# Performance work log

Measured on AMD Instinct MI355X. Metric: run time of the kernel, lower is better.

Reference implementation:

```python
import jax, jax.numpy as jnp
import numpy as np

C = 768      # n_embd
H = 12       # n_head
L = 6        # n_layer (per stack: base and head)
BS = 256     # block_size (per-stream length t)
B = 2        # batch
VU = 512     # vocab_size_up
VD = 512     # vocab_size_down
NM = 438     # n_music


def _ln(x, g, b, eps=1e-5):
    m = jnp.mean(x, -1, keepdims=True)
    v = jnp.mean((x - m) ** 2, -1, keepdims=True)
    return (x - m) * jax.lax.rsqrt(v + eps) * g + b


def _blocks(x, p, mask):
    # p: tuple of 16 stacked [L, ...] param arrays; scan over layers
    def body(x, lp):
        g1, b1, Wq, Bq, Wk, Bk, Wv, Bv, Wo, Bo, g2, b2, Wf, Bf, Wp, Bp = lp
        Bb, T, Cc = x.shape
        D = Cc // H
        h = _ln(x, g1, b1)
        q = (h @ Wq + Bq).reshape(Bb, T, H, D).transpose(0, 2, 1, 3)
        k = (h @ Wk + Bk).reshape(Bb, T, H, D).transpose(0, 2, 1, 3)
        v = (h @ Wv + Bv).reshape(Bb, T, H, D).transpose(0, 2, 1, 3)
        att = jnp.einsum('bhid,bhjd->bhij', q, k) * (1.0 / np.sqrt(D).astype(np.float32))
        att = jnp.where(mask, att, jnp.float32(-1e9))
        att = jax.nn.softmax(att, axis=-1)
        y = jnp.einsum('bhij,bhjd->bhid', att, v).transpose(0, 2, 1, 3).reshape(Bb, T, Cc)
        x = x + y @ Wo + Bo
        h2 = _ln(x, g2, b2)
        x = x + jax.nn.gelu(h2 @ Wf + Bf, approximate=False) @ Wp + Bp
        return x, None
    x, _ = jax.lax.scan(body, x, p)
    return x


def _forward(idx_up, idx_down, cond, tok_emb_up, tok_emb_down, pos_emb, cond_w, cond_b,
             base_p, head_p, ln_f_g, ln_f_b, head_up_w, head_down_w):
    t = idx_up.shape[1]
    te = jnp.concatenate([cond @ cond_w + cond_b, tok_emb_up[idx_up], tok_emb_down[idx_down]], axis=1)
    pe = jnp.concatenate([pos_emb[:, :t], pos_emb[:, BS:BS + t], pos_emb[:, 2 * BS:2 * BS + t]], axis=1)
    x = te + pe  # [B, 3t, C]
    tril = jnp.tril(jnp.ones((t, t), bool))
    mask = jnp.tile(tril, (3, 3))[None, None]  # 3x3 tiled block-causal mask [1,1,3t,3t]
    x = _blocks(x, base_p, mask)
    x = _blocks(x, head_p, mask)
    x = _ln(x, ln_f_g, ln_f_b)
    logits_up = x[:, t:2 * t] @ head_up_w
    logits_down = x[:, 2 * t:3 * t] @ head_down_w
    return logits_up, logits_down


def setup_inputs() -> dict:
    key = jax.random.key(0)
    ks = iter(jax.random.split(key, 100))
    def nrm(shape):
        return 0.02 * jax.random.normal(next(ks), shape, jnp.float32)
    inp = {
        'idx_up': jax.random.randint(next(ks), (B, BS), 0, VU),
        'idx_down': jax.random.randint(next(ks), (B, BS), 0, VD),
        'cond': jax.random.normal(next(ks), (B, BS, NM), jnp.float32),
        'tok_emb_up': nrm((VU, C)),
        'tok_emb_down': nrm((VD, C)),
        'pos_emb': nrm((1, 3 * BS, C)),
        'cond_w': nrm((NM, C)),
        'cond_b': jnp.zeros((C,), jnp.float32),
    }
    for pre in ('base_', 'head_'):
        inp[pre + 'ln1_g'] = jnp.ones((L, C), jnp.float32)
        inp[pre + 'ln1_b'] = jnp.zeros((L, C), jnp.float32)
        inp[pre + 'wq'] = nrm((L, C, C)); inp[pre + 'bq'] = jnp.zeros((L, C), jnp.float32)
        inp[pre + 'wk'] = nrm((L, C, C)); inp[pre + 'bk'] = jnp.zeros((L, C), jnp.float32)
        inp[pre + 'wv'] = nrm((L, C, C)); inp[pre + 'bv'] = jnp.zeros((L, C), jnp.float32)
        inp[pre + 'wo'] = nrm((L, C, C)); inp[pre + 'bo'] = jnp.zeros((L, C), jnp.float32)
        inp[pre + 'ln2_g'] = jnp.ones((L, C), jnp.float32)
        inp[pre + 'ln2_b'] = jnp.zeros((L, C), jnp.float32)
        inp[pre + 'fc_w'] = nrm((L, C, 4 * C)); inp[pre + 'fc_b'] = jnp.zeros((L, 4 * C), jnp.float32)
        inp[pre + 'pr_w'] = nrm((L, 4 * C, C)); inp[pre + 'pr_b'] = jnp.zeros((L, C), jnp.float32)
    inp['ln_f_g'] = jnp.ones((C,), jnp.float32)
    inp['ln_f_b'] = jnp.zeros((C,), jnp.float32)
    inp['head_up_w'] = nrm((C, VU))
    inp['head_down_w'] = nrm((C, VD))
    return inp


def reference(idx_up, idx_down, cond, tok_emb_up, tok_emb_down, pos_emb, cond_w, cond_b,
              base_ln1_g, base_ln1_b, base_wq, base_bq, base_wk, base_bk, base_wv, base_bv,
              base_wo, base_bo, base_ln2_g, base_ln2_b, base_fc_w, base_fc_b, base_pr_w, base_pr_b,
              head_ln1_g, head_ln1_b, head_wq, head_bq, head_wk, head_bk, head_wv, head_bv,
              head_wo, head_bo, head_ln2_g, head_ln2_b, head_fc_w, head_fc_b, head_pr_w, head_pr_b,
              ln_f_g, ln_f_b, head_up_w, head_down_w):
    base_p = (base_ln1_g, base_ln1_b, base_wq, base_bq, base_wk, base_bk, base_wv, base_bv,
              base_wo, base_bo, base_ln2_g, base_ln2_b, base_fc_w, base_fc_b, base_pr_w, base_pr_b)
    head_p = (head_ln1_g, head_ln1_b, head_wq, head_bq, head_wk, head_bk, head_wv, head_bv,
              head_wo, head_bo, head_ln2_g, head_ln2_b, head_fc_w, head_fc_b, head_pr_w, head_pr_b)
    return _forward(idx_up, idx_down, cond, tok_emb_up, tok_emb_down, pos_emb, cond_w, cond_b,
                    base_p, head_p, ln_f_g, ln_f_b, head_up_w, head_down_w)
```

## Files before the change

### kernel.cpp

```cpp
#include <hip/hip_runtime.h>
#include <cmath>

typedef unsigned short u16;
typedef __bf16 bf16x8 __attribute__((ext_vector_type(8)));
typedef float f32x4 __attribute__((ext_vector_type(4)));
typedef float f32x16 __attribute__((ext_vector_type(16)));
typedef u16 u16x4 __attribute__((ext_vector_type(4)));
typedef u16 u16x2 __attribute__((ext_vector_type(2)));

#define GLOAD16(g, l) __builtin_amdgcn_global_load_lds( \
    (const __attribute__((address_space(1))) unsigned int*)(g), \
    (__attribute__((address_space(3))) unsigned int*)(l), 16, 0, 0)

__device__ __forceinline__ u16 f2b(float f) {
  unsigned u = __builtin_bit_cast(unsigned, f);
  unsigned r = (u + 0x7fffu + ((u >> 16) & 1u)) >> 16;
  return (u16)r;
}

__device__ __forceinline__ int xcd_swz(int lin, int nwg) {
  int q = nwg >> 3, r = nwg & 7;
  int xcd = lin & 7, idx = lin >> 3;
  return xcd * q + (xcd < r ? xcd : r) + idx;
}

__global__ __launch_bounds__(256)
void transw_k(const float* __restrict__ W, u16* __restrict__ Wt,
              int K, int N, int Kp, long sIn, long sOut)
{
  __shared__ float t[32][33];
  int n0 = blockIdx.x * 32, k0 = blockIdx.y * 32, l = blockIdx.z;
  const float* Wl = W + (long)l * sIn;
  u16* Wo = Wt + (long)l * sOut;
  int tx = threadIdx.x & 31, ty = threadIdx.x >> 5;
  #pragma unroll
  for (int i = 0; i < 4; ++i) {
    int k = k0 + ty + i * 8;
    t[ty + i * 8][tx] = (k < K) ? Wl[(long)k * N + n0 + tx] : 0.0f;
  }
  __syncthreads();
  #pragma unroll
  for (int i = 0; i < 2; ++i) {
    int p = threadIdx.x + 256 * i;
    int nl = p >> 4, kk = (p & 15) * 2;
    u16x2 o2; o2[0] = f2b(t[kk][nl]); o2[1] = f2b(t[kk + 1][nl]);
    *(u16x2*)(Wo + (long)(n0 + nl) * Kp + k0 + kk) = o2;
  }
}

__global__ void biascat_k(const float* bq0, const float* bk0, const float* bv0,
                          const float* bq1, const float* bk1, const float* bv1, float* o)
{
  int idx = blockIdx.x * 256 + threadIdx.x;
  int c = idx % 2304, l = idx / 2304;
  int st = l / 6, li = l % 6;
  const float* src = (c < 768) ? (st ? bq1 : bq0) : (c < 1536) ? (st ? bk1 : bk0) : (st ? bv1 : bv0);
  o[idx] = src[li * 768 + (c % 768)];
}

__global__ void condcvt_k(const float* __restrict__ c, u16* __restrict__ o)
{
  int idx = blockIdx.x * 256 + threadIdx.x;
  int k = idx % 448, r = idx / 448;
  o[idx] = f2b(k < 438 ? c[r * 438 + k] : 0.0f);
}

__global__ void embed_k(const int* __restrict__ iu, const int* __restrict__ idn,
                        const float* __restrict__ teu, const float* __restrict__ ted,
                        const float* __restrict__ pe, float* __restrict__ x)
{
  int idx = blockIdx.x * 256 + threadIdx.x;
  int c4 = idx % 192; int rest = idx / 192;
  int tt = rest % 512; int b = rest / 512;
  int i = tt & 255; int s = tt >> 8;
  int tok = s ? idn[b * 256 + i] : iu[b * 256 + i];
  const float4* src = (const float4*)(s ? (ted + (long)tok * 768) : (teu + (long)tok * 768));
  int prow = 256 + s * 256 + i;
  float4 pv = ((const float4*)(pe + (long)prow * 768))[c4];
  float4 sv = src[c4];
  float4 ov; ov.x = sv.x + pv.x; ov.y = sv.y + pv.y; ov.z = sv.z + pv.z; ov.w = sv.w + pv.w;
  ((float4*)(x + ((long)b * 768 + prow) * 768))[c4] = ov;
}

template<int S, bool WX>
__global__ __launch_bounds__(256)
void lnred_k(const float* __restrict__ xin, const float* __restrict__ P,
             const float* __restrict__ bias, const float* __restrict__ gg,
             const float* __restrict__ bb, float* __restrict__ xout,
             u16* __restrict__ h)
{
  int row = blockIdx.x * 4 + (threadIdx.x >> 6);
  int lane = threadIdx.x & 63;
  long base = (long)row * 768;
  const float4* xr4 = (const float4*)(xin + base);
  float4 v[3]; float s = 0.0f;
  #pragma unroll
  for (int j = 0; j < 3; ++j) {
    int f = lane + 64 * j;
    float4 val = xr4[f];
    if (S > 0) {
      float4 bv = ((const float4*)bias)[f];
      val.x += bv.x; val.y += bv.y; val.z += bv.z; val.w += bv.w;
      #pragma unroll
      for (int si = 0; si < S; ++si) {
        float4 pv = ((const float4*)(P + (long)si * 1179648 + base))[f];
        val.x += pv.x; val.y += pv.y; val.z += pv.z; val.w += pv.w;
      }
    }
    if (WX) ((float4*)(xout + base))[f] = val;
    v[j] = val; s += val.x + val.y + val.z + val.w;
  }
  #pragma unroll
  for (int d = 1; d < 64; d <<= 1) s += __shfl_xor(s, d);
  float mean = s * (1.0f / 768.0f);
  float s2 = 0.0f;
  #pragma unroll
  for (int j = 0; j < 3; ++j) {
    float dx = v[j].x - mean, dy = v[j].y - mean, dz = v[j].z - mean, dw = v[j].w - mean;
    s2 += dx * dx + dy * dy + dz * dz + dw * dw;
  }
  #pragma unroll
  for (int d = 1; d < 64; d <<= 1) s2 += __shfl_xor(s2, d);
  float rstd = rsqrtf(s2 * (1.0f / 768.0f) + 1e-5f);
  u16* orow = h + base;
  #pragma unroll
  for (int j = 0; j < 3; ++j) {
    int f = lane + 64 * j;
    float4 gv = ((const float4*)gg)[f];
    float4 bv2 = ((const float4*)bb)[f];
    u16x4 pk;
    pk[0] = f2b((v[j].x - mean) * rstd * gv.x + bv2.x);
    pk[1] = f2b((v[j].y - mean) * rstd * gv.y + bv2.y);
    pk[2] = f2b((v[j].z - mean) * rstd * gv.z + bv2.z);
    pk[3] = f2b((v[j].w - mean) * rstd * gv.w + bv2.w);
    *(u16x4*)(orow + 4 * f) = pk;
  }
}

__global__ __launch_bounds__(256)
void headred_k(const float* __restrict__ HP, float* __restrict__ out)
{
  int i4 = blockIdx.x * 256 + threadIdx.x;
  int st = i4 >> 16, loc = i4 & 65535;
  int r = loc >> 7, c4 = loc & 127;
  const float4* basep = (const float4*)HP + (long)r * 256 + st * 128 + c4;
  float4 a = basep[0], b = basep[131072], c = basep[2 * 131072], d = basep[3 * 131072];
  float4 rr; rr.x = a.x + b.x + c.x + d.x; rr.y = a.y + b.y + c.y + d.y;
  rr.z = a.z + b.z + c.z + d.z; rr.w = a.w + b.w + c.w + d.w;
  ((float4*)out)[i4] = rr;
}

#define EPI_PLAIN 0
#define EPI_PE    1
#define EPI_QKV   2
#define EPI_GELU  4
#define EPI_PART  5
#define EPI_HEAD  6

template<int BM, int BN, int WM, int WN, int EPI, bool BIAS>
__global__ __launch_bounds__(256)
void gemm_k(const u16* __restrict__ A, const u16* __restrict__ Bt, const float* __restrict__ bias,
            float* outf, u16* outb, u16* qb, u16* kb, u16* vT, const float* aux,
            int M, int N, int Ks, int lda, int ldb, int ldc,
            int astr, int aoff, int cstr, int coff, int pstr)
{
  constexpr int NWC = BN / WN;
  constexpr int NT  = (BM / WM) * NWC * 64;
  constexpr int LCH = (BM + BN) * 8;
  constexpr int LPT = LCH / NT;
  constexpr int MR = WM / 32, NR = WN / 32;
  __shared__ alignas(16) u16 Sl[2][(BM + BN) * 64];

  const int tid = threadIdx.x;
  const int gx = gridDim.x, gy = gridDim.y;
  const int nwg = gx * gy * gridDim.z;
  const int lin = (blockIdx.z * gy + blockIdx.y) * gx + blockIdx.x;
  const int wg = xcd_swz(lin, nwg);
  const int bx = wg % gx, t1g = wg / gx;
  const int by = t1g % gy, bz = t1g / gy;
  const int m0 = bx * BM, n0 = by * BN;
  const int koff = bz * Ks;
  const int lane = tid & 63, w = tid >> 6;
  const int l31 = lane & 31, hl = lane >> 5;
  const int wr = w / NWC, wc = w % NWC;
  int aoffE = aoff;
  if constexpr (EPI == EPI_HEAD) aoffE += (by >= (int)(gy >> 1)) ? 256 : 0;

  const u16* gp[LPT]; int lbase[LPT];
  #pragma unroll
  for (int j = 0; j < LPT; ++j) {
    int c = tid + NT * j;
    int slot = c & 7;
    if (c < BM * 8) {
      int row = c >> 3;
      int se = (slot ^ (row & 7)) * 8;
      int am = m0 + row;
      gp[j] = A + (long)((am >> 8) * astr + aoffE + (am & 255)) * lda + koff + se;
    } else {
      int rb = c - BM * 8;
      int row = rb >> 3;
      int se = (slot ^ (row & 7)) * 8;
      gp[j] = Bt + (long)(n0 + row) * ldb + koff + se;
    }
    lbase[j] = w * 512 + NT * 8 * j;
  }

  int offA[4][MR], offB[4][NR];
  #pragma unroll
  for (int kst = 0; kst < 4; ++kst) {
    int s = 2 * kst + hl;
    #pragma unroll
    for (int mi = 0; mi < MR; ++mi) {
      int r = wr * WM + mi * 32 + l31;
      offA[kst][mi] = r * 128 + ((s ^ (r & 7)) << 4);
    }
    #pragma unroll
    for (int ni = 0; ni < NR; ++ni) {
      int r = wc * WN + ni * 32 + l31;
      offB[kst][ni] = BM * 128 + r * 128 + ((s ^ (r & 7)) << 4);
    }
  }

  f32x16 acc[MR][NR];
  #pragma unroll
  for (int mi = 0; mi < MR; ++mi)
  #pragma unroll
  for (int ni = 0; ni < NR; ++ni) acc[mi][ni] = f32x16{};

  auto STAGE = [&](int kt, int buf) {
    #pragma unroll
    for (int j = 0; j < LPT; ++j) GLOAD16(gp[j] + kt, &Sl[buf][lbase[j]]);
  };
  auto COMPUTE = [&](int buf) {
    const char* Sb = (const char*)&Sl[buf][0];
    #pragma unroll
    for (int kst = 0; kst < 4; ++kst) {
      bf16x8 a[MR], b[NR];
      #pragma unroll
      for (int mi = 0; mi < MR; ++mi) a[mi] = *(const bf16x8*)(Sb + offA[kst][mi]);
      #pragma unroll
      for (int ni = 0; ni < NR; ++ni) b[ni] = *(const bf16x8*)(Sb + offB[kst][ni]);
      #pragma unroll
      for (int mi = 0; mi < MR; ++mi)
      #pragma unroll
      for (int ni = 0; ni < NR; ++ni)
        acc[mi][ni] = __builtin_amdgcn_mfma_f32_32x32x16_bf16(a[mi], b[ni], acc[mi][ni], 0, 0, 0);
    }
  };

  const int nIter = Ks >> 6;
  STAGE(0, 0);
  if (nIter > 1) STAGE(64, 1);
  for (int t = 0; t < nIter; ++t) {
    if (t + 1 < nIter) {
      if constexpr (LPT == 8)      asm volatile("s_waitcnt vmcnt(8)" ::: "memory");
      else if constexpr (LPT == 6) asm volatile("s_waitcnt vmcnt(6)" ::: "memory");
      else                         asm volatile("s_waitcnt vmcnt(4)" ::: "memory");
    } else {
      asm volatile("s_waitcnt vmcnt(0)" ::: "memory");
    }
    __builtin_amdgcn_s_barrier();
    COMPUTE(t & 1);
    if (t + 2 < nIter) {
      __builtin_amdgcn_s_barrier();
      STAGE((t + 2) << 6, t & 1);
    }
  }

  #pragma unroll
  for (int mi = 0; mi < MR; ++mi)
  #pragma unroll
  for (int ni = 0; ni < NR; ++ni) {
    f32x16 a = acc[mi][ni];
    int col = n0 + wc * WN + ni * 32 + l31;
    float bv = BIAS ? bias[col] : 0.0f;
    int mlb = m0 + wr * WM + mi * 32 + 4 * hl;
    if constexpr (EPI == EPI_QKV) {
      if (col >= 1536) {
        int c2 = col - 1536, hh = c2 >> 6, dd = c2 & 63;
        #pragma unroll
        for (int q = 0; q < 4; ++q) {
          int t0r = mlb + 8 * q;
          int bb2 = t0r >= 768 ? 1 : 0;
          int t0 = t0r - bb2 * 768;
          u16x4 pk;
          #pragma unroll
          for (int r = 0; r < 4; ++r) pk[r] = f2b(a[4 * q + r] + bv);
          *(u16x4*)(vT + (long)((bb2 * 12 + hh) * 64 + dd) * 768 + t0) = pk;
        }
      } else {
        u16* dst = (col < 768) ? (qb + col) : (kb + (col - 768));
        #pragma unroll
        for (int q = 0; q < 4; ++q)
        #pragma unroll
        for (int r = 0; r < 4; ++r) {
          int row = mlb + 8 * q + r;
          dst[(long)row * 768] = f2b(a[4 * q + r] + bv);
        }
      }
    } else {
      #pragma unroll
      for (int q = 0; q < 4; ++q)
      #pragma unroll
      for (int r = 0; r < 4; ++r) {
        int rg = mlb + 8 * q + r;
        long crow = (long)(rg >> 8) * cstr + coff + (rg & 255);
        float v = a[4 * q + r] + bv;
        if (EPI == EPI_PLAIN)      outf[crow * ldc + col] = v;
        else if (EPI == EPI_PE)    outf[crow * ldc + col] = v + aux[(long)(rg & 255) * 768 + col];
        else if (EPI == EPI_PART || EPI == EPI_HEAD)
                                   outf[(long)bz * pstr + (long)rg * ldc + col] = v;
        else if (EPI == EPI_GELU)  outb[crow * ldc + col] = f2b(0.5f * v * (1.0f + erff(v * 0.70710678f)));
      }
    }
  }
}

#define MFMA_BF16 __builtin_amdgcn_mfma_f32_16x16x32_bf16
__global__ __launch_bounds__(128)
void attn_k(const u16* __restrict__ qb, const u16* __restrict__ kb,
            const u16* __restrict__ vT, u16* __restrict__ y)
{
  __shared__ alignas(16) u16 Kl[3 * 4096];
  __shared__ alignas(16) u16 Vl[3 * 4096];
  __shared__ alignas(16) u16 Pl[2][16 * 72];
  const int gx = gridDim.x, gy = gridDim.y;
  const int nwg = gx * gy;
  const int lin = blockIdx.y * gx + blockIdx.x;
  const int wg = xcd_swz(lin, nwg);
  const int qt = wg % gx, bh = wg / gx;
  const int b = bh / 12, h = bh - b * 12;
  const int tid = threadIdx.x, w = tid >> 6, lane = tid & 63, l15 = lane & 15, g = lane >> 4;
  const int qrow = qt * 32 + w * 16 + l15;
  const int qm = qrow & 255;
  const int q0 = (qt * 32) & 255;
  const unsigned nw4 = (q0 >> 6) + 1;
  const int niter = 3 * nw4;
  const u16* qp = qb + (long)(b * 768 + qrow) * 768 + h * 64;
  bf16x8 qf0 = *(const bf16x8*)(qp + 8 * g);
  bf16x8 qf1 = *(const bf16x8*)(qp + 32 + 8 * g);
  f32x4 O0{}, O1{}, O2{}, O3{};
  float m_run = -1e30f, l_run = 0.0f;

  const u16* kp[4]; const u16* vp[4]; int ldsb[4];
  #pragma unroll
  for (int j = 0; j < 4; ++j) {
    int i = tid + 128 * j;
    int r = i >> 3, sl = ((i & 7) ^ (r & 7)) * 8;
    kp[j] = kb + (long)(b * 768 + r) * 768 + h * 64 + sl;
    vp[j] = vT + (long)(bh * 64 + r) * 768 + sl;
    ldsb[j] = (w + 2 * j) * 512;
  }

  auto STAGE = [&](int kt, int q) {
    u16* kd = Kl + q * 4096; u16* vd = Vl + q * 4096;
    #pragma unroll
    for (int j = 0; j < 4; ++j) GLOAD16(kp[j] + (long)kt * 64 * 768, kd + ldsb[j]);
    #pragma unroll
    for (int j = 0; j < 4; ++j) GLOAD16(vp[j] + kt * 64, vd + ldsb[j]);
  };
  auto MAP = [&](int it) {
    unsigned sb = (unsigned)it / nw4;
    return (int)(sb * 4 + ((unsigned)it - sb * nw4));
  };

  STAGE(MAP(0), 0);
  STAGE(MAP(1), 1);
  int cur = 0;
  for (int it = 0; it < niter; ++it) {
    if (it < niter - 1) asm volatile("s_waitcnt vmcnt(8)" ::: "memory");
    else                asm volatile("s_waitcnt vmcnt(0)" ::: "memory");
    __builtin_amdgcn_s_barrier();
    if (it + 2 < niter) STAGE(MAP(it + 2), cur == 0 ? 2 : cur - 1);
    const int kt = MAP(it);
    const char* Kb = (const char*)Kl + cur * 8192;
    const char* Vb = (const char*)Vl + cur * 8192;

    f32x4 s0{}, s1{}, s2{}, s3{};
    #pragma unroll
    for (int ks = 0; ks < 2; ++ks) {
      bf16x8 qf = ks ? qf1 : qf0;
      int sb = ((4 * ks + g) ^ (l15 & 7)) << 4;
      bf16x8 k0 = *(const bf16x8*)(Kb + (0  + l15) * 128 + sb);
      bf16x8 k1 = *(const bf16x8*)(Kb + (16 + l15) * 128 + sb);
      bf16x8 k2 = *(const bf16x8*)(Kb + (32 + l15) * 128 + sb);
      bf16x8 k3 = *(const bf16x8*)(Kb + (48 + l15) * 128 + sb);
      s0 = MFMA_BF16(k0, qf, s0, 0, 0, 0);
      s1 = MFMA_BF16(k1, qf, s1, 0, 0, 0);
      s2 = MFMA_BF16(k2, qf, s2, 0, 0, 0);
      s3 = MFMA_BF16(k3, qf, s3, 0, 0, 0);
    }
    float sv[16]; float tm = -1e30f;
    #pragma unroll
    for (int mt = 0; mt < 4; ++mt) {
      f32x4 sm4 = (mt == 0) ? s0 : (mt == 1) ? s1 : (mt == 2) ? s2 : s3;
      #pragma unroll
      for (int r = 0; r < 4; ++r) {
        int kg = kt * 64 + mt * 16 + 4 * g + r;
        float val = ((kg & 255) <= qm) ? sm4[r] * 0.125f : -1e30f;
        sv[mt * 4 + r] = val; tm = fmaxf(tm, val);
      }
    }
    tm = fmaxf(tm, __shfl_xor(tm, 16));
    tm = fmaxf(tm, __shfl_xor(tm, 32));
    float mn = fmaxf(m_run, tm);
    float alpha = __expf(m_run - mn);
    float ps = 0.0f; u16 pb16[16];
    #pragma unroll
    for (int j = 0; j < 16; ++j) {
      float p = (sv[j] <= -1e29f) ? 0.0f : __expf(sv[j] - mn);
      ps += p; pb16[j] = f2b(p);
    }
    ps += __shfl_xor(ps, 16); ps += __shfl_xor(ps, 32);
    l_run = l_run * alpha + ps; m_run = mn;
    float a0 = __shfl(alpha, 4 * g + 0);
    float a1 = __shfl(alpha, 4 * g + 1);
    float a2 = __shfl(alpha, 4 * g + 2);
    float a3 = __shfl(alpha, 4 * g + 3);
    #pragma unroll
    for (int mt = 0; mt < 4; ++mt) {
      u16x4 pk; pk[0] = pb16[4*mt]; pk[1] = pb16[4*mt+1]; pk[2] = pb16[4*mt+2]; pk[3] = pb16[4*mt+3];
      *(u16x4*)((char*)&Pl[w][0] + l15 * 144 + mt * 32 + 8 * g) = pk;
    }
    O0[0] *= a0; O0[1] *= a1; O0[2] *= a2; O0[3] *= a3;
    O1[0] *= a0; O1[1] *= a1; O1[2] *= a2; O1[3] *= a3;
    O2[0] *= a0; O2[1] *= a1; O2[2] *= a2; O2[3] *= a3;
    O3[0] *= a0; O3[1] *= a1; O3[2] *= a2; O3[3] *= a3;
    asm volatile("s_waitcnt lgkmcnt(0)" ::: "memory");
    __builtin_amdgcn_sched_barrier(0);
    #pragma unroll
    for (int ks = 0; ks < 2; ++ks) {
      bf16x8 pf = *(const bf16x8*)((const char*)&Pl[w][0] + l15 * 144 + 64 * ks + 16 * g);
      int sb = ((4 * ks + g) ^ (l15 & 7)) << 4;
      bf16x8 v0 = *(const bf16x8*)(Vb + (0  + l15) * 128 + sb);
      bf16x8 v1 = *(const bf16x8*)(Vb + (16 + l15) * 128 + sb);
      bf16x8 v2 = *(const bf16x8*)(Vb + (32 + l15) * 128 + sb);
      bf16x8 v3 = *(const bf16x8*)(Vb + (48 + l15) * 128 + sb);
      O0 = MFMA_BF16(pf, v0, O0, 0, 0, 0);
      O1 = MFMA_BF16(pf, v1, O1, 0, 0, 0);
      O2 = MFMA_BF16(pf, v2, O2, 0, 0, 0);
      O3 = MFMA_BF16(pf, v3, O3, 0, 0, 0);
    }
    cur = (cur == 2) ? 0 : cur + 1;
  }
  float n0i = 1.0f / __shfl(l_run, 4 * g + 0);
  float n1i = 1.0f / __shfl(l_run, 4 * g + 1);
  float n2i = 1.0f / __shfl(l_run, 4 * g + 2);
  float n3i = 1.0f / __shfl(l_run, 4 * g + 3);
  long yr = (long)(b * 768 + qt * 32 + w * 16 + 4 * g);
  #pragma unroll
  for (int ni = 0; ni < 4; ++ni) {
    f32x4 Ov = (ni == 0) ? O0 : (ni == 1) ? O1 : (ni == 2) ? O2 : O3;
    int c = h * 64 + ni * 16 + l15;
    y[(yr + 0) * 768 + c] = f2b(Ov[0] * n0i);
    y[(yr + 1) * 768 + c] = f2b(Ov[1] * n1i);
    y[(yr + 2) * 768 + c] = f2b(Ov[2] * n2i);
    y[(yr + 3) * 768 + c] = f2b(Ov[3] * n3i);
  }
}

extern "C" void kernel_launch(void* const* d_in, const int* in_sizes, int n_in,
                              void* d_out, int out_size, void* d_ws, size_t ws_size,
                              hipStream_t stream)
{
  (void)in_sizes; (void)n_in; (void)out_size;
  auto F = [&](int i){ return (const float*)d_in[i]; };
  const int* idx_up = (const int*)d_in[0];
  const int* idx_dn = (const int*)d_in[1];
  const float* cond = F(2);
  const float* teu = F(3);
  const float* ted = F(4);
  const float* pe  = F(5);
  const float* cw  = F(6);
  const float* cb  = F(7);
  float* outp = (float*)d_out;
  char* ws = (char*)d_ws;

  size_t o = 0;
  auto take = [&](size_t bytes){ void* p = ws + o; o += bytes; return p; };
  float* x    = (float*)take(4718592);
  u16*   h    = (u16*)take(2359296);
  u16*   qbuf = (u16*)take(2359296);
  u16*   kbuf = (u16*)take(2359296);
  u16*   vT   = (u16*)take(2359296);
  u16*   y    = (u16*)take(2359296);
  u16*   fca  = (u16*)take(9437184);
  u16*   xf   = (u16*)take(2359296);
  u16*   cbf  = (u16*)take(458752);
  float* qkvb = (float*)take(110592);
  u16*   hutd = (u16*)take(1572864);
  u16*   cwt  = (u16*)take(688128);
  float* P1   = (float*)take(9437184);
  float* P2   = (float*)take(9437184);
  float* HP   = (float*)take(8388608);
  const size_t WL = 14155776;
  bool up = (ws_size >= o + 12 * WL);
  size_t nsl = up ? 12 : 1;
  u16* qkvt = (u16*)(ws + o);
  u16* wot  = qkvt + nsl * 2304 * 768;
  u16* fct  = wot  + nsl * 768 * 768;
  u16* prt  = fct  + nsl * 3072 * 768;

  auto trans = [&](const float* src, u16* dst, int K, int N, int Kp, long sIn, long sOut, int nz){
    transw_k<<<dim3(N / 32, Kp / 32, nz), dim3(256), 0, stream>>>(src, dst, K, N, Kp, sIn, sOut);
  };

  if (up) {
    for (int s = 0; s < 2; ++s) {
      for (int p = 0; p < 3; ++p)
        trans(F(8 + 16*s + 2 + 2*p), qkvt + (size_t)s*6*2304*768 + (size_t)p*768*768,
              768, 768, 768, 768L*768, 2304L*768, 6);
      trans(F(8 + 16*s + 8),  wot + (size_t)s*6*768*768,  768, 768, 768, 768L*768, 768L*768, 6);
      trans(F(8 + 16*s + 12), fct + (size_t)s*6*3072*768, 768, 3072, 768, 768L*3072, 3072L*768, 6);
      trans(F(8 + 16*s + 14), prt + (size_t)s*6*768*3072, 3072, 768, 3072, 3072L*768, 768L*3072, 6);
    }
  }
  trans(F(42), hutd, 768, 512, 768, 0, 0, 1);
  trans(F(43), hutd + 512 * 768, 768, 512, 768, 0, 0, 1);
  trans(cw,    cwt, 438, 768, 448, 0, 0, 1);
  biascat_k<<<dim3(108), dim3(256), 0, stream>>>(F(11), F(13), F(15), F(27), F(29), F(31), qkvb);
  condcvt_k<<<dim3(896), dim3(256), 0, stream>>>(cond, cbf);
  embed_k<<<dim3(768), dim3(256), 0, stream>>>(idx_up, idx_dn, teu, ted, pe, x);
  gemm_k<64, 64, 32, 32, EPI_PE, true><<<dim3(8, 12, 1), dim3(256), 0, stream>>>(cbf, cwt, cb,
      x, nullptr, nullptr, nullptr, nullptr, pe,
      512, 768, 448, 448, 448, 768, 256, 0, 768, 0, 0);

  for (int l = 0; l < 12; ++l) {
    int s = l / 6, li = l % 6;
    u16* qkvt_l = qkvt + (up ? (size_t)l : 0) * 2304 * 768;
    u16* wot_l  = wot  + (up ? (size_t)l : 0) * 768 * 768;
    u16* fct_l  = fct  + (up ? (size_t)l : 0) * 3072 * 768;
    u16* prt_l  = prt  + (up ? (size_t)l : 0) * 768 * 3072;
    if (!up) {
      for (int p = 0; p < 3; ++p)
        trans(F(8 + 16*s + 2 + 2*p) + (size_t)li*768*768, qkvt_l + (size_t)p*768*768, 768, 768, 768, 0, 0, 1);
      trans(F(8 + 16*s + 8)  + (size_t)li*768*768,  wot_l, 768, 768, 768, 0, 0, 1);
      trans(F(8 + 16*s + 12) + (size_t)li*768*3072, fct_l, 768, 3072, 768, 0, 0, 1);
      trans(F(8 + 16*s + 14) + (size_t)li*3072*768, prt_l, 3072, 768, 3072, 0, 0, 1);
    }
    if (l == 0) {
      lnred_k<0, false><<<dim3(384), dim3(256), 0, stream>>>(x, nullptr, nullptr,
          F(8+16*s+0) + (size_t)li*768, F(8+16*s+1) + (size_t)li*768, nullptr, h);
    } else {
      int ps = (l - 1) / 6, pli = (l - 1) % 6;
      lnred_k<2, true><<<dim3(384), dim3(256), 0, stream>>>(x, P2,
          F(8+16*ps+15) + (size_t)pli*768,
          F(8+16*s+0) + (size_t)li*768, F(8+16*s+1) + (size_t)li*768, x, h);
    }
    gemm_k<128, 64, 32, 64, EPI_QKV, true><<<dim3(12, 36, 1), dim3(256), 0, stream>>>(h, qkvt_l, qkvb + (size_t)l*2304,
        nullptr, nullptr, qbuf, kbuf, vT, nullptr,
        1536, 2304, 768, 768, 768, 768, 256, 0, 256, 0, 0);
    attn_k<<<dim3(24, 24), dim3(128), 0, stream>>>(qbuf, kbuf, vT, y);
    gemm_k<128, 64, 32, 64, EPI_PART, false><<<dim3(12, 12, 2), dim3(256), 0, stream>>>(y, wot_l, nullptr,
        P1, nullptr, nullptr, nullptr, nullptr, nullptr,
        1536, 768, 384, 768, 768, 768, 256, 0, 256, 0, 1179648);
    lnred_k<2, true><<<dim3(384), dim3(256), 0, stream>>>(x, P1,
        F(8+16*s+9) + (size_t)li*768,
        F(8+16*s+10) + (size_t)li*768, F(8+16*s+11) + (size_t)li*768, x, h);
    gemm_k<128, 64, 32, 64, EPI_GELU, true><<<dim3(12, 48, 1), dim3(256), 0, stream>>>(h, fct_l, F(8+16*s+13) + (size_t)li*3072,
        nullptr, fca, nullptr, nullptr, nullptr, nullptr,
        1536, 3072, 768, 768, 768, 3072, 256, 0, 256, 0, 0);
    gemm_k<128, 64, 32, 64, EPI_PART, false><<<dim3(12, 12, 2), dim3(256), 0, stream>>>(fca, prt_l, nullptr,
        P2, nullptr, nullptr, nullptr, nullptr, nullptr,
        1536, 768, 1536, 3072, 3072, 768, 256, 0, 256, 0, 1179648);
  }
  lnred_k<2, false><<<dim3(384), dim3(256), 0, stream>>>(x, P2,
      F(8+16*1+15) + (size_t)5*768, F(40), F(41), nullptr, xf);
  gemm_k<64, 64, 32, 32, EPI_HEAD, false><<<dim3(8, 16, 4), dim3(256), 0, stream>>>(xf, hutd, nullptr,
      HP, nullptr, nullptr, nullptr, nullptr, nullptr,
      512, 1024, 192, 768, 768, 1024, 768, 256, 256, 0, 524288);
  headred_k<<<dim3(512), dim3(256), 0, stream>>>(HP, outp);
}
```

Measured before the change: 1.311 ms.

## Batch weight transposes into one launch and triple-buffer GEMM LDS stages

All per-stack weight transpose/convert launches are merged into a single kernel driven by a job table. Each block finds its job by a linear scan over the job bases. The GEMM main loop moves from two LDS buffers to three, so the prefetch of tile t+2 is issued before computing tile t and the second barrier per iteration is dropped. This cuts launch overhead and improves load/compute overlap, at the cost of 50% more LDS per block, which may reduce occupancy.

```diff
diff --git a/kernel.cpp b/kernel.cpp
--- a/kernel.cpp
+++ b/kernel.cpp
@@ -24,19 +24,19 @@
   return xcd * q + (xcd < r ? xcd : r) + idx;
 }
 
-__global__ __launch_bounds__(256)
-void transw_k(const float* __restrict__ W, u16* __restrict__ Wt,
-              int K, int N, int Kp, long sIn, long sOut)
+#define MAXTJ 80
+struct TJob { const float* src; u16* dst; int K, N, Kp, base; };
+struct TJobs { TJob j[MAXTJ]; int nj; };
+
+__device__ __forceinline__ void trans_tile(const float* __restrict__ W, u16* __restrict__ Wo,
+                                           int K, int N, int Kp, int n0, int k0)
 {
   __shared__ float t[32][33];
-  int n0 = blockIdx.x * 32, k0 = blockIdx.y * 32, l = blockIdx.z;
-  const float* Wl = W + (long)l * sIn;
-  u16* Wo = Wt + (long)l * sOut;
   int tx = threadIdx.x & 31, ty = threadIdx.x >> 5;
   #pragma unroll
   for (int i = 0; i < 4; ++i) {
     int k = k0 + ty + i * 8;
-    t[ty + i * 8][tx] = (k < K) ? Wl[(long)k * N + n0 + tx] : 0.0f;
+    t[ty + i * 8][tx] = (k < K) ? W[(long)k * N + n0 + tx] : 0.0f;
   }
   __syncthreads();
   #pragma unroll
@@ -46,6 +46,27 @@
     u16x2 o2; o2[0] = f2b(t[kk][nl]); o2[1] = f2b(t[kk + 1][nl]);
     *(u16x2*)(Wo + (long)(n0 + nl) * Kp + k0 + kk) = o2;
   }
+}
+
+__global__ __launch_bounds__(256)
+void transb_k(TJobs P)
+{
+  int bid = blockIdx.x;
+  int lo = 0;
+  for (int i = 1; i < P.nj; ++i) if (P.j[i].base <= bid) lo = i;
+  TJob J = P.j[lo];
+  int local = bid - J.base;
+  int tilesX = J.N >> 5;
+  int n0 = (local % tilesX) * 32, k0 = (local / tilesX) * 32;
+  trans_tile(J.src, J.dst, J.K, J.N, J.Kp, n0, k0);
+}
+
+__global__ __launch_bounds__(256)
+void transw_k(const float* __restrict__ W, u16* __restrict__ Wt,
+              int K, int N, int Kp, long sIn, long sOut)
+{
+  int l = blockIdx.z;
+  trans_tile(W + (long)l * sIn, Wt + (long)l * sOut, K, N, Kp, blockIdx.x * 32, blockIdx.y * 32);
 }
 
 __global__ void biascat_k(const float* bq0, const float* bk0, const float* bv0,
@@ -169,7 +190,7 @@
   constexpr int LCH = (BM + BN) * 8;
   constexpr int LPT = LCH / NT;
   constexpr int MR = WM / 32, NR = WN / 32;
-  __shared__ alignas(16) u16 Sl[2][(BM + BN) * 64];
+  __shared__ alignas(16) u16 Sl[3][(BM + BN) * 64];
 
   const int tid = threadIdx.x;
   const int gx = gridDim.x, gy = gridDim.y;
@@ -251,6 +272,7 @@
   const int nIter = Ks >> 6;
   STAGE(0, 0);
   if (nIter > 1) STAGE(64, 1);
+  int cur = 0;
   for (int t = 0; t < nIter; ++t) {
     if (t + 1 < nIter) {
       if constexpr (LPT == 8)      asm volatile("s_waitcnt vmcnt(8)" ::: "memory");
@@ -260,11 +282,12 @@
       asm volatile("s_waitcnt vmcnt(0)" ::: "memory");
     }
     __builtin_amdgcn_s_barrier();
-    COMPUTE(t & 1);
     if (t + 2 < nIter) {
-      __builtin_amdgcn_s_barrier();
-      STAGE((t + 2) << 6, t & 1);
-    }
+      int nslot = cur + 2; if (nslot >= 3) nslot -= 3;
+      STAGE((t + 2) << 6, nslot);
+    }
+    COMPUTE(cur);
+    ++cur; if (cur == 3) cur = 0;
   }
 
   #pragma unroll
@@ -506,18 +529,32 @@
   };
 
   if (up) {
-    for (int s = 0; s < 2; ++s) {
-      for (int p = 0; p < 3; ++p)
-        trans(F(8 + 16*s + 2 + 2*p), qkvt + (size_t)s*6*2304*768 + (size_t)p*768*768,
-              768, 768, 768, 768L*768, 2304L*768, 6);
-      trans(F(8 + 16*s + 8),  wot + (size_t)s*6*768*768,  768, 768, 768, 768L*768, 768L*768, 6);
-      trans(F(8 + 16*s + 12), fct + (size_t)s*6*3072*768, 768, 3072, 768, 768L*3072, 3072L*768, 6);
-      trans(F(8 + 16*s + 14), prt + (size_t)s*6*768*3072, 3072, 768, 3072, 3072L*768, 768L*3072, 6);
-    }
-  }
-  trans(F(42), hutd, 768, 512, 768, 0, 0, 1);
-  trans(F(43), hutd + 512 * 768, 768, 512, 768, 0, 0, 1);
-  trans(cw,    cwt, 438, 768, 448, 0, 0, 1);
+    TJobs P; int nt = 0, nj = 0;
+    auto addjob = [&](const float* src, u16* dst, int K, int N, int Kp) {
+      P.j[nj].src = src; P.j[nj].dst = dst;
+      P.j[nj].K = K; P.j[nj].N = N; P.j[nj].Kp = Kp; P.j[nj].base = nt;
+      nt += (N >> 5) * (Kp >> 5); ++nj;
+    };
+    for (int s = 0; s < 2; ++s)
+      for (int li = 0; li < 6; ++li) {
+        size_t l = s * 6 + li;
+        for (int p = 0; p < 3; ++p)
+          addjob(F(8 + 16*s + 2 + 2*p) + (size_t)li*768*768,
+                 qkvt + l*2304*768 + (size_t)p*768*768, 768, 768, 768);
+        addjob(F(8 + 16*s + 8)  + (size_t)li*768*768,  wot + l*768*768,  768, 768, 768);
+        addjob(F(8 + 16*s + 12) + (size_t)li*768*3072, fct + l*3072*768, 768, 3072, 768);
+        addjob(F(8 + 16*s + 14) + (size_t)li*3072*768, prt + l*768*3072, 3072, 768, 3072);
+      }
+    addjob(F(42), hutd,            768, 512, 768);
+    addjob(F(43), hutd + 512*768,  768, 512, 768);
+    addjob(cw,    cwt,             438, 768, 448);
+    P.nj = nj;
+    transb_k<<<dim3(nt), dim3(256), 0, stream>>>(P);
+  } else {
+    trans(F(42), hutd, 768, 512, 768, 0, 0, 1);
+    trans(F(43), hutd + 512 * 768, 768, 512, 768, 0, 0, 1);
+    trans(cw,    cwt, 438, 768, 448, 0, 0, 1);
+  }
   biascat_k<<<dim3(108), dim3(256), 0, stream>>>(F(11), F(13), F(15), F(27), F(29), F(31), qkvb);
   condcvt_k<<<dim3(896), dim3(256), 0, stream>>>(cond, cbf);
   embed_k<<<dim3(768), dim3(256), 0, stream>>>(idx_up, idx_dn, teu, ted, pe, x);
```

Measured after the change: 1.590 ms. 1.21x slower.
